# Optimization experiments

Measured on AMD Instinct MI355X. Metric: run time of the kernel, lower is better.

The kernel has to match this reference:

```python
import jax, jax.numpy as jnp
import numpy as np
from jax import lax

ACT_SCALE = (0.5, 0.5, 0.5)  # act_scale[0..2], also used as bias_scale
STRIDE = 2
QLEVELS = 127.0  # int8 fake-quant levels (2**7 - 1)


@jax.custom_vjp
def ste_round(x):
    return jnp.round(x)

def _ste_fwd(x):
    return jnp.round(x), None

def _ste_bwd(_, g):
    return (g,)

ste_round.defvjp(_ste_fwd, _ste_bwd)


def fq_act(x, scale):
    # quantize_activations_gemm_A: normalize by scale, clip to [-1,1], 8-bit grid
    return ste_round(jnp.clip(x / scale, -1.0, 1.0) * QLEVELS) / QLEVELS


def qw(w):
    # quantize_weight_gemm_S: per-tensor max-abs scale + 8-bit fake quant
    s = jnp.max(jnp.abs(w))
    wq = ste_round(jnp.clip(w / s, -1.0, 1.0) * QLEVELS) / QLEVELS
    return wq, s


def qb(b):
    # quantize_bias_gemm: round to 1/127 grid
    return ste_round(b * QLEVELS) / QLEVELS


def relu6s(x, scale):
    # ReLU6S: scaled ReLU6
    return jnp.clip(x / scale, 0.0, 6.0)


def conv(x, w, stride=1, pad=0):
    return lax.conv_general_dilated(
        x, w, (stride, stride), [(pad, pad), (pad, pad)],
        dimension_numbers=("NCHW", "OIHW", "NCHW"))


def bottleneck_fwd(x, w1, b1, w2, b2, w3, b3, ws, bs):
    s0, s1, s2a = ACT_SCALE
    x = fq_act(x, s0)
    residual = x
    # conv1: 1x1
    w1q, c1s = qw(w1)
    b1q = qb(b1) / (c1s * s0)
    out = (conv(x, w1q) + b1q[None, :, None, None]) * c1s
    out = relu6s(out, s0) * s0
    out = fq_act(out, s1)
    # conv2: 3x3 stride
    w2q, c2s = qw(w2)
    b2q = qb(b2) / (c2s * s1)
    out = (conv(out, w2q, stride=STRIDE, pad=1) + b2q[None, :, None, None]) * c2s
    out = relu6s(out, s1) * s1
    out = fq_act(out, s2a)
    # conv3: 1x1 (source's padding=1 on a 1x1 conv is a shape bug; dropped)
    w3q, c3s = qw(w3)
    b3q = qb(b3) / (c2s * s2a)  # NOTE: source divides by conv2_scale (preserved)
    out = (conv(out, w3q) + b3q[None, :, None, None]) * c3s
    out = out * s2a
    # downsample shortcut: 1x1 stride
    wsq, css = qw(ws)
    bsq = qb(bs) / (css * s0)
    residual = (conv(residual, wsq, stride=STRIDE) + bsq[None, :, None, None]) * css
    residual = residual * s0
    return jnp.clip(out + residual, 0.0, 6.0)  # final ReLU6


def setup_inputs() -> dict:
    key = jax.random.key(0)
    ks = jax.random.split(key, 9)
    B, Cin, P, H, W = 64, 512, 256, 28, 28
    Cout = 4 * P
    def w_init(k, shape):
        fan_in = shape[1] * shape[2] * shape[3]
        return jax.random.normal(k, shape, jnp.float32) * np.float32(np.sqrt(2.0 / fan_in))
    return {
        "x": jax.random.normal(ks[0], (B, Cin, H, W), jnp.float32),
        "w1": w_init(ks[1], (P, Cin, 1, 1)),
        "b1": jax.random.normal(ks[2], (P,), jnp.float32) * 0.01,
        "w2": w_init(ks[3], (P, P, 3, 3)),
        "b2": jax.random.normal(ks[4], (P,), jnp.float32) * 0.01,
        "w3": w_init(ks[5], (Cout, P, 1, 1)),
        "b3": jax.random.normal(ks[6], (Cout,), jnp.float32) * 0.01,
        "ws": w_init(ks[7], (Cout, Cin, 1, 1)),
        "bs": jax.random.normal(ks[8], (Cout,), jnp.float32) * 0.01,
    }


def reference(x, w1, b1, w2, b2, w3, b3, ws, bs):
    return bottleneck_fwd(x, w1, b1, w2, b2, w3, b3, ws, bs)
```

## Files before the change

kernel.cpp:

```cpp
#include <hip/hip_runtime.h>
#include <stdint.h>

typedef int   int4v __attribute__((ext_vector_type(4)));
typedef float f32x4 __attribute__((ext_vector_type(4)));

#define WS_SCALES 0ull
#define WS_ZERO   256ull
#define WS_BI1    1024ull
#define WS_BI2    2048ull
#define WS_BI3    4096ull
#define WS_BIS    8192ull
#define WS_W1Q    16384ull
#define WS_W2Q    (WS_W1Q + 131072ull)
#define WS_W3Q    (WS_W2Q + 589824ull)
#define WS_WSQ    (WS_W3Q + 262144ull)
#define WS_A0     2097152ull
#define WS_A1     (WS_A0 + 25690112ull)
#define WS_A2     (WS_A1 + 12845056ull)

__device__ __forceinline__ void gll16(const void* g, void* l) {
    __builtin_amdgcn_global_load_lds((const __attribute__((address_space(1))) void*)g,
                                     (__attribute__((address_space(3))) void*)l, 16, 0, 0);
}

#define VMCNT_BAR(n) asm volatile("s_waitcnt vmcnt(" #n ")\n\ts_barrier" ::: "memory")

__global__ void k_init(float* wshead) {
    int i = blockIdx.x * 256 + threadIdx.x;
    wshead[i] = 0.0f;
}

__global__ void k_maxabs(const float* __restrict__ w1, const float* __restrict__ w2,
                         const float* __restrict__ w3, const float* __restrict__ wsd,
                         float* __restrict__ scales) {
    const float* srcs[4] = {w1, w2, w3, wsd};
    const int ns[4] = {131072, 589824, 262144, 524288};
    int t = blockIdx.y;
    const float* s = srcs[t];
    int n = ns[t];
    float m = 0.0f;
    for (int i = blockIdx.x * 256 + threadIdx.x; i < n; i += gridDim.x * 256)
        m = fmaxf(m, fabsf(s[i]));
    __shared__ float red[256];
    red[threadIdx.x] = m;
    __syncthreads();
    for (int st = 128; st > 0; st >>= 1) {
        if (threadIdx.x < st) red[threadIdx.x] = fmaxf(red[threadIdx.x], red[threadIdx.x + st]);
        __syncthreads();
    }
    if (threadIdx.x == 0) atomicMax((int*)&scales[t], __float_as_int(red[0]));
}

__global__ void k_quant_w(const float* __restrict__ w1, const float* __restrict__ w2,
                          const float* __restrict__ w3, const float* __restrict__ wsd,
                          const float* __restrict__ b1, const float* __restrict__ b2,
                          const float* __restrict__ b3, const float* __restrict__ bs,
                          char* __restrict__ wsb) {
    const float* sc = (const float*)(wsb + WS_SCALES);
    int mode = blockIdx.y;
    int i0 = blockIdx.x * 256 + threadIdx.x;
    int stride = gridDim.x * 256;
    if (mode == 0) {
        float s = sc[0]; signed char* o = (signed char*)(wsb + WS_W1Q);
        for (int i = i0; i < 131072; i += stride)
            o[i] = (signed char)(int)rintf(fminf(fmaxf(w1[i] / s, -1.f), 1.f) * 127.f);
    } else if (mode == 1) {
        float s = sc[1]; signed char* o = (signed char*)(wsb + WS_W2Q);
        for (int i = i0; i < 589824; i += stride) {
            int oo = i / 2304, r2 = i - oo * 2304;
            int c = r2 / 9, kk = r2 - c * 9;
            o[(size_t)oo * 2304 + kk * 256 + c] =
                (signed char)(int)rintf(fminf(fmaxf(w2[i] / s, -1.f), 1.f) * 127.f);
        }
    } else if (mode == 2) {
        float s = sc[2]; signed char* o = (signed char*)(wsb + WS_W3Q);
        for (int i = i0; i < 262144; i += stride)
            o[i] = (signed char)(int)rintf(fminf(fmaxf(w3[i] / s, -1.f), 1.f) * 127.f);
    } else if (mode == 3) {
        float s = sc[3]; signed char* o = (signed char*)(wsb + WS_WSQ);
        for (int i = i0; i < 524288; i += stride)
            o[i] = (signed char)(int)rintf(fminf(fmaxf(wsd[i] / s, -1.f), 1.f) * 127.f);
    } else if (mode == 4) {
        float* o = (float*)(wsb + WS_BI1);
        for (int i = i0; i < 256; i += stride) o[i] = rintf(b1[i] * 127.f);
    } else if (mode == 5) {
        float* o = (float*)(wsb + WS_BI2);
        for (int i = i0; i < 256; i += stride) o[i] = rintf(b2[i] * 127.f);
    } else if (mode == 6) {
        float* o = (float*)(wsb + WS_BI3);
        for (int i = i0; i < 1024; i += stride) o[i] = rintf(b3[i] * 127.f);
    } else {
        float* o = (float*)(wsb + WS_BIS);
        for (int i = i0; i < 1024; i += stride) o[i] = rintf(bs[i] * 127.f);
    }
}

__global__ void k_quant_x(const float* __restrict__ x, signed char* __restrict__ a0) {
    __shared__ signed char tile[32][33];
    int b = blockIdx.z;
    int p0 = blockIdx.x * 32, c0 = blockIdx.y * 32;
    int tp = threadIdx.x & 31, tr = threadIdx.x >> 5;
    const float* xb = x + ((size_t)b * 512 + c0) * 784 + p0;
    for (int i = 0; i < 4; i++) {
        int cc = tr + i * 8;
        float v = (p0 + tp < 784) ? xb[(size_t)cc * 784 + tp] : 0.f;
        v = fminf(fmaxf(v * 2.f, -1.f), 1.f);
        tile[cc][tp] = (signed char)(int)rintf(v * 127.f);
    }
    __syncthreads();
    int pp = threadIdx.x >> 3, cs = (threadIdx.x & 7) * 4;
    if (p0 + pp < 784) {
        unsigned pk = 0;
        for (int i = 0; i < 4; i++)
            pk |= (unsigned)(unsigned char)tile[cs + i][pp] << (8 * i);
        *(unsigned*)(a0 + ((size_t)b * 784 + p0 + pp) * 512 + c0 + cs) = pk;
    }
}

template <int MODE, int BM, int BN, int WGM, int WGN>
__global__ __launch_bounds__(256) void k_conv(char* __restrict__ wsb, float* __restrict__ dout) {
    constexpr int FM = BM / WGM / 16;
    constexpr int FN = BN / WGN / 16;
    constexpr int ISS_A = BM / 16;
    constexpr int NISS = (BM + BN) / 16;
    constexpr int NI = NISS / 4;
    constexpr int KTOT = (MODE == 0) ? 512 : (MODE == 1) ? 2304 : 768;
    constexpr int NSTEP = KTOT / 64;
    constexpr int BMP = BM + 16;
    constexpr int LDS_STAGE = (BM + BN) * 64;
    constexpr int LDS_EPI = (MODE == 2) ? 64 * (BN + 4) * 4 : BN * BMP;
    constexpr int LDSZ = (3 * LDS_STAGE > LDS_EPI) ? 3 * LDS_STAGE : LDS_EPI;

    __shared__ alignas(16) char lds[LDSZ];

    const int tid = threadIdx.x;
    const int wid = tid >> 6;
    const int lane = tid & 63;
    const int n0 = blockIdx.x * BN;
    const int m0 = blockIdx.y * BM;
    const int bb = blockIdx.z;

    const float* sc = (const float*)(wsb + WS_SCALES);
    const int srow = lane >> 2;
    const int lrow = lane & 15;
    const int quad = lane >> 4;
    const int wm = (wid % WGM) * (BM / WGM);
    const int wn = (wid / WGM) * (BN / WGN);
    const int xco = ((lane & 3) ^ ((lane >> 3) & 3)) << 4;
    const char* zp = wsb + WS_ZERO + xco;

    int4v acc3[FM][FN] = {};
    int4v accS[FM][FN] = {};

    auto src_ptr = [&](int s, int k0) -> const char* {
        const char* g;
        if (s < ISS_A) {
            int m = m0 + s * 16 + srow;
            if (MODE == 0)
                g = wsb + WS_W1Q + (size_t)m * 512 + k0 + xco;
            else if (MODE == 1)
                g = wsb + WS_W2Q + (size_t)m * 2304 + k0 + xco;
            else
                g = (k0 < 256) ? wsb + WS_W3Q + (size_t)m * 256 + k0 + xco
                               : wsb + WS_WSQ + (size_t)m * 512 + (k0 - 256) + xco;
        } else {
            int n = n0 + (s - ISS_A) * 16 + srow;
            g = zp;
            if (MODE == 0) {
                g = wsb + WS_A0 + (size_t)n * 512 + k0 + xco;
            } else if (MODE == 1) {
                unsigned b = (unsigned)n / 196u;
                unsigned hw = (unsigned)n - b * 196u;
                int oh = hw / 14, ow = hw - oh * 14;
                int tap = k0 >> 8;
                int kh = tap / 3, kw = tap - kh * 3;
                int c0 = k0 & 255;
                int ih = 2 * oh - 1 + kh, iw = 2 * ow - 1 + kw;
                if (ih >= 0 && ih < 28 && iw >= 0 && iw < 28)
                    g = wsb + WS_A1 + ((size_t)b * 784 + ih * 28 + iw) * 256 + c0 + xco;
            } else {
                if (n < 196) {
                    if (k0 < 256) {
                        g = wsb + WS_A2 + ((size_t)bb * 196 + n) * 256 + k0 + xco;
                    } else {
                        int oh = n / 14, ow = n - oh * 14;
                        int ps = oh * 56 + ow * 2;
                        g = wsb + WS_A0 + ((size_t)bb * 784 + ps) * 512 + (k0 - 256) + xco;
                    }
                }
            }
        }
        return g;
    };

    auto stage = [&](int t, char* buf) {
        const int k0 = t * 64;
#pragma unroll
        for (int ii = 0; ii < NI; ii++) {
            const int s = wid + ii * 4;
            gll16(src_ptr(s, k0), buf + s * 1024);
        }
    };

    stage(0, lds);
    stage(1, lds + LDS_STAGE);
    for (int t = 0; t < NSTEP; ++t) {
        char* cur = lds + (t % 3) * LDS_STAGE;
        if (t == NSTEP - 1) {
            VMCNT_BAR(0);
        } else if constexpr (NI == 3) {
            VMCNT_BAR(3);
        } else {
            VMCNT_BAR(4);
        }
        if (t + 2 < NSTEP) stage(t + 2, lds + ((t + 2) % 3) * LDS_STAGE);

        int4v afr[FM], bfr[FN];
#pragma unroll
        for (int i = 0; i < FM; i++) {
            int m = wm + i * 16 + lrow;
            afr[i] = *(const int4v*)(cur + m * 64 + ((quad ^ ((m >> 1) & 3)) << 4));
        }
#pragma unroll
        for (int j = 0; j < FN; j++) {
            int n = wn + j * 16 + lrow;
            bfr[j] = *(const int4v*)(cur + (BM + n) * 64 + ((quad ^ ((n >> 1) & 3)) << 4));
        }
        if (MODE != 2 || t < 4) {
#pragma unroll
            for (int i = 0; i < FM; i++)
#pragma unroll
                for (int j = 0; j < FN; j++)
                    acc3[i][j] = __builtin_amdgcn_mfma_i32_16x16x64_i8(afr[i], bfr[j], acc3[i][j], 0, 0, 0);
        } else {
#pragma unroll
            for (int i = 0; i < FM; i++)
#pragma unroll
                for (int j = 0; j < FN; j++)
                    accS[i][j] = __builtin_amdgcn_mfma_i32_16x16x64_i8(afr[i], bfr[j], accS[i][j], 0, 0, 0);
        }
    }

    if (MODE == 0 || MODE == 1) {
        const float alpha = sc[MODE] / 16129.0f;
        const float* bi = (const float*)(wsb + (MODE == 0 ? WS_BI1 : WS_BI2));
        signed char* outp = (signed char*)(wsb + (MODE == 0 ? WS_A1 : WS_A2));
        __syncthreads();
#pragma unroll
        for (int i = 0; i < FM; i++) {
            int mloc = wm + i * 16 + quad * 4;
            int mb = m0 + mloc;
            float bt[4];
#pragma unroll
            for (int r = 0; r < 4; r++) bt[r] = bi[mb + r] * (2.0f / 127.0f);
#pragma unroll
            for (int j = 0; j < FN; j++) {
                int nloc = wn + j * 16 + lrow;
                unsigned pk = 0;
#pragma unroll
                for (int r = 0; r < 4; r++) {
                    float v = alpha * (float)acc3[i][j][r] + bt[r];
                    int q = (int)rintf(127.0f * fminf(fmaxf(2.0f * v, 0.0f), 1.0f));
                    pk |= (unsigned)(q & 0xFF) << (8 * r);
                }
                *(unsigned*)(lds + nloc * BMP + mloc) = pk;
            }
        }
        __syncthreads();
        for (int u = tid; u < BN * (BM / 16); u += 256) {
            int row = u / (BM / 16);
            int seg = u % (BM / 16);
            uint4 v = *(const uint4*)(lds + row * BMP + seg * 16);
            *(uint4*)(outp + (size_t)(n0 + row) * 256 + m0 + seg * 16) = v;
        }
    } else {
        const float c2 = sc[1], c3 = sc[2], cS = sc[3];
        const float* bi3 = (const float*)(wsb + WS_BI3);
        const float* bis = (const float*)(wsb + WS_BIS);
        float* ldsF = (float*)lds;
        constexpr int LDN = BN + 4;
        constexpr int SEGS = BN / 16;
        for (int half = 0; half < 2; half++) {
            __syncthreads();
            if (wm == half * 64) {
#pragma unroll
                for (int i = 0; i < FM; i++) {
                    int mloc = i * 16 + quad * 4;
                    int mg = m0 + half * 64 + mloc;
                    float bt[4];
#pragma unroll
                    for (int r = 0; r < 4; r++)
                        bt[r] = bi3[mg + r] * (c3 / (127.0f * c2)) + bis[mg + r] * (1.0f / 127.0f);
#pragma unroll
                    for (int j = 0; j < FN; j++) {
                        int nloc = wn + j * 16 + lrow;
#pragma unroll
                        for (int r = 0; r < 4; r++) {
                            float v = (c3 * (float)acc3[i][j][r] + cS * (float)accS[i][j][r])
                                          * (0.5f / 16129.0f) + bt[r];
                            v = v < 0.0f ? 0.0f : (v > 6.0f ? 6.0f : v);
                            ldsF[(mloc + r) * LDN + nloc] = v;
                        }
                    }
                }
            }
            __syncthreads();
            {
                int rw0 = tid / SEGS, seg = tid % SEGS;
                int nbase = n0 + seg * 16;
                for (int row = rw0; row < 64; row += 256 / SEGS) {
                    const float* src = ldsF + row * LDN + seg * 16;
                    float* dst = dout + ((size_t)bb * 1024 + m0 + half * 64 + row) * 196 + nbase;
                    if (nbase + 16 <= 196) {
                        *(f32x4*)(dst + 0)  = *(const f32x4*)(src + 0);
                        *(f32x4*)(dst + 4)  = *(const f32x4*)(src + 4);
                        *(f32x4*)(dst + 8)  = *(const f32x4*)(src + 8);
                        *(f32x4*)(dst + 12) = *(const f32x4*)(src + 12);
                    } else {
                        for (int q = 0; q < 16 && nbase + q < 196; q++) dst[q] = src[q];
                    }
                }
            }
        }
    }
}

extern "C" void kernel_launch(void* const* d_in, const int* in_sizes, int n_in,
                              void* d_out, int out_size, void* d_ws, size_t ws_size,
                              hipStream_t stream) {
    const float* x   = (const float*)d_in[0];
    const float* w1  = (const float*)d_in[1];
    const float* b1  = (const float*)d_in[2];
    const float* w2  = (const float*)d_in[3];
    const float* b2  = (const float*)d_in[4];
    const float* w3  = (const float*)d_in[5];
    const float* b3  = (const float*)d_in[6];
    const float* wsd = (const float*)d_in[7];
    const float* bs  = (const float*)d_in[8];
    float* out = (float*)d_out;
    char* wsb = (char*)d_ws;

    k_init<<<16, 256, 0, stream>>>((float*)wsb);
    k_maxabs<<<dim3(32, 4), 256, 0, stream>>>(w1, w2, w3, wsd, (float*)(wsb + WS_SCALES));
    k_quant_w<<<dim3(96, 8), 256, 0, stream>>>(w1, w2, w3, wsd, b1, b2, b3, bs, wsb);
    k_quant_x<<<dim3(25, 16, 64), 256, 0, stream>>>(x, (signed char*)(wsb + WS_A0));
    k_conv<0, 128, 128, 2, 2><<<dim3(392, 2, 1), 256, 0, stream>>>(wsb, out);
    k_conv<1, 64, 128, 2, 2><<<dim3(98, 4, 1), 256, 0, stream>>>(wsb, out);
    k_conv<2, 128, 128, 2, 2><<<dim3(2, 8, 64), 256, 0, stream>>>(wsb, out);
}
```

Measured before the change: 328.7 us.

## Load conv weights directly to registers, vectorize quant_x and maxabs

The conv kernels no longer stage the weight (A) operand through LDS. Each wave now loads its A fragments straight from global memory into registers, double-buffered across an unrolled-by-two K loop, and only the activation (B) tiles go through the LDS triple buffer. This cuts LDS footprint and global-to-LDS traffic, at the cost of more registers and uncoalesced 16-byte global loads per lane. Separately, k_quant_x is widened to 128 pixels per block with float4 loads, and k_maxabs uses float4 loads over a larger grid, to reduce memory instruction overhead in the preprocessing.

```diff
diff --git a/kernel.cpp b/kernel.cpp
--- a/kernel.cpp
+++ b/kernel.cpp
@@ -34,13 +34,15 @@
                          const float* __restrict__ w3, const float* __restrict__ wsd,
                          float* __restrict__ scales) {
     const float* srcs[4] = {w1, w2, w3, wsd};
-    const int ns[4] = {131072, 589824, 262144, 524288};
+    const int n4s[4] = {32768, 147456, 65536, 131072};
     int t = blockIdx.y;
-    const float* s = srcs[t];
-    int n = ns[t];
+    const f32x4* s = (const f32x4*)srcs[t];
+    int n4 = n4s[t];
     float m = 0.0f;
-    for (int i = blockIdx.x * 256 + threadIdx.x; i < n; i += gridDim.x * 256)
-        m = fmaxf(m, fabsf(s[i]));
+    for (int i = blockIdx.x * 256 + threadIdx.x; i < n4; i += gridDim.x * 256) {
+        f32x4 v = s[i];
+        m = fmaxf(m, fmaxf(fmaxf(fabsf(v[0]), fabsf(v[1])), fmaxf(fabsf(v[2]), fabsf(v[3]))));
+    }
     __shared__ float red[256];
     red[threadIdx.x] = m;
     __syncthreads();
@@ -95,25 +97,39 @@
     }
 }
 
-__global__ void k_quant_x(const float* __restrict__ x, signed char* __restrict__ a0) {
-    __shared__ signed char tile[32][33];
+__global__ __launch_bounds__(256) void k_quant_x(const float* __restrict__ x,
+                                                 signed char* __restrict__ a0) {
+    __shared__ signed char tile[32][132];
     int b = blockIdx.z;
-    int p0 = blockIdx.x * 32, c0 = blockIdx.y * 32;
-    int tp = threadIdx.x & 31, tr = threadIdx.x >> 5;
-    const float* xb = x + ((size_t)b * 512 + c0) * 784 + p0;
-    for (int i = 0; i < 4; i++) {
-        int cc = tr + i * 8;
-        float v = (p0 + tp < 784) ? xb[(size_t)cc * 784 + tp] : 0.f;
-        v = fminf(fmaxf(v * 2.f, -1.f), 1.f);
-        tile[cc][tp] = (signed char)(int)rintf(v * 127.f);
+    int p0 = blockIdx.x * 128, c0 = blockIdx.y * 32;
+    int tc = threadIdx.x >> 3;
+    int pq = (threadIdx.x & 7) * 16;
+    const float* xr = x + ((size_t)b * 512 + c0 + tc) * 784 + p0 + pq;
+#pragma unroll
+    for (int u = 0; u < 4; u++) {
+        int p = p0 + pq + u * 4;
+        f32x4 v = {0.f, 0.f, 0.f, 0.f};
+        if (p < 784) v = *(const f32x4*)(xr + u * 4);
+        signed char q[4];
+#pragma unroll
+        for (int e = 0; e < 4; e++) {
+            float f = fminf(fmaxf(v[e] * 2.f, -1.f), 1.f);
+            q[e] = (signed char)(int)rintf(f * 127.f);
+        }
+        *(int*)&tile[tc][pq + u * 4] = *(int*)q;
     }
     __syncthreads();
-    int pp = threadIdx.x >> 3, cs = (threadIdx.x & 7) * 4;
-    if (p0 + pp < 784) {
-        unsigned pk = 0;
-        for (int i = 0; i < 4; i++)
-            pk |= (unsigned)(unsigned char)tile[cs + i][pp] << (8 * i);
-        *(unsigned*)(a0 + ((size_t)b * 784 + p0 + pp) * 512 + c0 + cs) = pk;
+#pragma unroll
+    for (int u = 0; u < 4; u++) {
+        int idx = threadIdx.x + u * 256;
+        int pp = idx >> 3, cs = (idx & 7) * 4;
+        if (p0 + pp < 784) {
+            unsigned pk = 0;
+#pragma unroll
+            for (int i = 0; i < 4; i++)
+                pk |= (unsigned)(unsigned char)tile[cs + i][pp] << (8 * i);
+            *(unsigned*)(a0 + ((size_t)b * 784 + p0 + pp) * 512 + c0 + cs) = pk;
+        }
     }
 }
 
@@ -121,15 +137,17 @@
 __global__ __launch_bounds__(256) void k_conv(char* __restrict__ wsb, float* __restrict__ dout) {
     constexpr int FM = BM / WGM / 16;
     constexpr int FN = BN / WGN / 16;
-    constexpr int ISS_A = BM / 16;
-    constexpr int NISS = (BM + BN) / 16;
-    constexpr int NI = NISS / 4;
+    constexpr int SB = BN / 16;
+    constexpr int NI_B = SB / 4;
     constexpr int KTOT = (MODE == 0) ? 512 : (MODE == 1) ? 2304 : 768;
     constexpr int NSTEP = KTOT / 64;
     constexpr int BMP = BM + 16;
-    constexpr int LDS_STAGE = (BM + BN) * 64;
+    constexpr int LDS_STAGE = BN * 64;
     constexpr int LDS_EPI = (MODE == 2) ? 64 * (BN + 4) * 4 : BN * BMP;
     constexpr int LDSZ = (3 * LDS_STAGE > LDS_EPI) ? 3 * LDS_STAGE : LDS_EPI;
+    static_assert(FM + NI_B == 6 || FM + NI_B == 4, "steady bar count");
+    static_assert(FM == 4 || FM == 2, "tail bar count");
+    static_assert(NSTEP % 2 == 0, "even steps");
 
     __shared__ alignas(16) char lds[LDSZ];
 
@@ -149,99 +167,125 @@
     const int xco = ((lane & 3) ^ ((lane >> 3) & 3)) << 4;
     const char* zp = wsb + WS_ZERO + xco;
 
+    const char* aB[FM];
+    const char* aB2[FM];
+#pragma unroll
+    for (int i = 0; i < FM; i++) {
+        int m = m0 + wm + i * 16 + lrow;
+        if constexpr (MODE == 0) {
+            aB[i] = wsb + WS_W1Q + (size_t)m * 512 + quad * 16;
+        } else if constexpr (MODE == 1) {
+            aB[i] = wsb + WS_W2Q + (size_t)m * 2304 + quad * 16;
+        } else {
+            aB[i]  = wsb + WS_W3Q + (size_t)m * 256 + quad * 16;
+            aB2[i] = wsb + WS_WSQ + (size_t)m * 512 + quad * 16;
+        }
+    }
+
     int4v acc3[FM][FN] = {};
     int4v accS[FM][FN] = {};
 
-    auto src_ptr = [&](int s, int k0) -> const char* {
-        const char* g;
-        if (s < ISS_A) {
-            int m = m0 + s * 16 + srow;
-            if (MODE == 0)
-                g = wsb + WS_W1Q + (size_t)m * 512 + k0 + xco;
-            else if (MODE == 1)
-                g = wsb + WS_W2Q + (size_t)m * 2304 + k0 + xco;
-            else
-                g = (k0 < 256) ? wsb + WS_W3Q + (size_t)m * 256 + k0 + xco
-                               : wsb + WS_WSQ + (size_t)m * 512 + (k0 - 256) + xco;
+    auto srcB = [&](int s, int k0) -> const char* {
+        int n = n0 + s * 16 + srow;
+        const char* g = zp;
+        if constexpr (MODE == 0) {
+            g = wsb + WS_A0 + (size_t)n * 512 + k0 + xco;
+        } else if constexpr (MODE == 1) {
+            unsigned b = (unsigned)n / 196u;
+            unsigned hw = (unsigned)n - b * 196u;
+            int oh = hw / 14, ow = hw - oh * 14;
+            int tap = k0 >> 8;
+            int kh = tap / 3, kw = tap - kh * 3;
+            int c0 = k0 & 255;
+            int ih = 2 * oh - 1 + kh, iw = 2 * ow - 1 + kw;
+            if (ih >= 0 && ih < 28 && iw >= 0 && iw < 28)
+                g = wsb + WS_A1 + ((size_t)b * 784 + ih * 28 + iw) * 256 + c0 + xco;
         } else {
-            int n = n0 + (s - ISS_A) * 16 + srow;
-            g = zp;
-            if (MODE == 0) {
-                g = wsb + WS_A0 + (size_t)n * 512 + k0 + xco;
-            } else if (MODE == 1) {
-                unsigned b = (unsigned)n / 196u;
-                unsigned hw = (unsigned)n - b * 196u;
-                int oh = hw / 14, ow = hw - oh * 14;
-                int tap = k0 >> 8;
-                int kh = tap / 3, kw = tap - kh * 3;
-                int c0 = k0 & 255;
-                int ih = 2 * oh - 1 + kh, iw = 2 * ow - 1 + kw;
-                if (ih >= 0 && ih < 28 && iw >= 0 && iw < 28)
-                    g = wsb + WS_A1 + ((size_t)b * 784 + ih * 28 + iw) * 256 + c0 + xco;
+            if (n < 196) {
+                if (k0 < 256) {
+                    g = wsb + WS_A2 + ((size_t)bb * 196 + n) * 256 + k0 + xco;
+                } else {
+                    int oh = n / 14, ow = n - oh * 14;
+                    int ps = oh * 56 + ow * 2;
+                    g = wsb + WS_A0 + ((size_t)bb * 784 + ps) * 512 + (k0 - 256) + xco;
+                }
+            }
+        }
+        return g;
+    };
+
+    auto stageB = [&](int t, char* buf) {
+        const int k0 = t * 64;
+#pragma unroll
+        for (int ii = 0; ii < NI_B; ii++) {
+            const int s = wid + ii * 4;
+            gll16(srcB(s, k0), buf + s * 1024);
+        }
+    };
+
+    auto loadA = [&](int t, int4v (&a)[FM]) {
+        if constexpr (MODE == 2) {
+            if (t < 4) {
+                const int off = t * 64;
+#pragma unroll
+                for (int i = 0; i < FM; i++) a[i] = *(const int4v*)(aB[i] + off);
             } else {
-                if (n < 196) {
-                    if (k0 < 256) {
-                        g = wsb + WS_A2 + ((size_t)bb * 196 + n) * 256 + k0 + xco;
-                    } else {
-                        int oh = n / 14, ow = n - oh * 14;
-                        int ps = oh * 56 + ow * 2;
-                        g = wsb + WS_A0 + ((size_t)bb * 784 + ps) * 512 + (k0 - 256) + xco;
-                    }
-                }
-            }
-        }
-        return g;
-    };
-
-    auto stage = [&](int t, char* buf) {
-        const int k0 = t * 64;
-#pragma unroll
-        for (int ii = 0; ii < NI; ii++) {
-            const int s = wid + ii * 4;
-            gll16(src_ptr(s, k0), buf + s * 1024);
-        }
-    };
-
-    stage(0, lds);
-    stage(1, lds + LDS_STAGE);
-    for (int t = 0; t < NSTEP; ++t) {
-        char* cur = lds + (t % 3) * LDS_STAGE;
-        if (t == NSTEP - 1) {
-            VMCNT_BAR(0);
-        } else if constexpr (NI == 3) {
-            VMCNT_BAR(3);
+                const int off = (t - 4) * 64;
+#pragma unroll
+                for (int i = 0; i < FM; i++) a[i] = *(const int4v*)(aB2[i] + off);
+            }
         } else {
-            VMCNT_BAR(4);
-        }
-        if (t + 2 < NSTEP) stage(t + 2, lds + ((t + 2) % 3) * LDS_STAGE);
-
-        int4v afr[FM], bfr[FN];
-#pragma unroll
-        for (int i = 0; i < FM; i++) {
-            int m = wm + i * 16 + lrow;
-            afr[i] = *(const int4v*)(cur + m * 64 + ((quad ^ ((m >> 1) & 3)) << 4));
-        }
+            const int off = t * 64;
+#pragma unroll
+            for (int i = 0; i < FM; i++) a[i] = *(const int4v*)(aB[i] + off);
+        }
+    };
+
+    auto dsB = [&](const char* cur, int4v (&b)[FN]) {
 #pragma unroll
         for (int j = 0; j < FN; j++) {
             int n = wn + j * 16 + lrow;
-            bfr[j] = *(const int4v*)(cur + (BM + n) * 64 + ((quad ^ ((n >> 1) & 3)) << 4));
-        }
-        if (MODE != 2 || t < 4) {
-#pragma unroll
-            for (int i = 0; i < FM; i++)
-#pragma unroll
-                for (int j = 0; j < FN; j++)
-                    acc3[i][j] = __builtin_amdgcn_mfma_i32_16x16x64_i8(afr[i], bfr[j], acc3[i][j], 0, 0, 0);
+            b[j] = *(const int4v*)(cur + n * 64 + ((quad ^ ((n >> 1) & 3)) << 4));
+        }
+    };
+
+    auto MF = [&](int4v (&ac)[FM][FN], int4v (&a)[FM], int4v (&b)[FN]) {
+#pragma unroll
+        for (int i = 0; i < FM; i++)
+#pragma unroll
+            for (int j = 0; j < FN; j++)
+                ac[i][j] = __builtin_amdgcn_mfma_i32_16x16x64_i8(a[i], b[j], ac[i][j], 0, 0, 0);
+    };
+
+    int4v aC[FM], aN[FM], bfr[FN];
+    stageB(0, lds);
+    stageB(1, lds + LDS_STAGE);
+    loadA(0, aC);
+    VMCNT_BAR(0);
+
+    for (int t = 0; t < NSTEP; t += 2) {
+        loadA(t + 1, aN);
+        __builtin_amdgcn_sched_barrier(0);
+        if (t + 2 < NSTEP) stageB(t + 2, lds + ((t + 2) % 3) * LDS_STAGE);
+        dsB(lds + (t % 3) * LDS_STAGE, bfr);
+        if (MODE != 2 || t < 4) MF(acc3, aC, bfr); else MF(accS, aC, bfr);
+        if (t + 1 == NSTEP - 1) {
+            if constexpr (FM == 4) VMCNT_BAR(4); else VMCNT_BAR(2);
         } else {
-#pragma unroll
-            for (int i = 0; i < FM; i++)
-#pragma unroll
-                for (int j = 0; j < FN; j++)
-                    accS[i][j] = __builtin_amdgcn_mfma_i32_16x16x64_i8(afr[i], bfr[j], accS[i][j], 0, 0, 0);
-        }
-    }
-
-    if (MODE == 0 || MODE == 1) {
+            if constexpr (FM + NI_B == 6) VMCNT_BAR(6); else VMCNT_BAR(4);
+        }
+
+        if (t + 2 < NSTEP) loadA(t + 2, aC);
+        __builtin_amdgcn_sched_barrier(0);
+        if (t + 3 < NSTEP) stageB(t + 3, lds + ((t + 3) % 3) * LDS_STAGE);
+        dsB(lds + ((t + 1) % 3) * LDS_STAGE, bfr);
+        if (MODE != 2 || t + 1 < 4) MF(acc3, aN, bfr); else MF(accS, aN, bfr);
+        if (t + 2 < NSTEP) {
+            if constexpr (FM + NI_B == 6) VMCNT_BAR(6); else VMCNT_BAR(4);
+        }
+    }
+
+    if constexpr (MODE == 0 || MODE == 1) {
         const float alpha = sc[MODE] / 16129.0f;
         const float* bi = (const float*)(wsb + (MODE == 0 ? WS_BI1 : WS_BI2));
         signed char* outp = (signed char*)(wsb + (MODE == 0 ? WS_A1 : WS_A2));
@@ -341,9 +385,9 @@
     char* wsb = (char*)d_ws;
 
     k_init<<<16, 256, 0, stream>>>((float*)wsb);
-    k_maxabs<<<dim3(32, 4), 256, 0, stream>>>(w1, w2, w3, wsd, (float*)(wsb + WS_SCALES));
+    k_maxabs<<<dim3(128, 4), 256, 0, stream>>>(w1, w2, w3, wsd, (float*)(wsb + WS_SCALES));
     k_quant_w<<<dim3(96, 8), 256, 0, stream>>>(w1, w2, w3, wsd, b1, b2, b3, bs, wsb);
-    k_quant_x<<<dim3(25, 16, 64), 256, 0, stream>>>(x, (signed char*)(wsb + WS_A0));
+    k_quant_x<<<dim3(7, 16, 64), 256, 0, stream>>>(x, (signed char*)(wsb + WS_A0));
     k_conv<0, 128, 128, 2, 2><<<dim3(392, 2, 1), 256, 0, stream>>>(wsb, out);
     k_conv<1, 64, 128, 2, 2><<<dim3(98, 4, 1), 256, 0, stream>>>(wsb, out);
     k_conv<2, 128, 128, 2, 2><<<dim3(2, 8, 64), 256, 0, stream>>>(wsb, out);
```

Measured after the change: 334.9 us. About the same (+1.9%).

## Shrink conv tiles to 64x64, vectorize maxabs and input quantization

Applied to the files above, without the earlier changes.

All three conv kernels now use 64x64 tiles with launch bounds of four blocks per CU. This multiplies the grid size to raise occupancy and simplifies the epilogues into single-pass stores. The maxabs and input-quantization kernels are vectorized with float4 loads, and quant_x now processes 128 pixels per block. The barrier macro also waits on lgkmcnt(0). Smaller tiles reduce data reuse per block and increase global and LDS traffic.

```diff
diff --git a/kernel.cpp b/kernel.cpp
--- a/kernel.cpp
+++ b/kernel.cpp
@@ -23,7 +23,7 @@
                                      (__attribute__((address_space(3))) void*)l, 16, 0, 0);
 }
 
-#define VMCNT_BAR(n) asm volatile("s_waitcnt vmcnt(" #n ")\n\ts_barrier" ::: "memory")
+#define VMCNT_BAR(n) asm volatile("s_waitcnt vmcnt(" #n ") lgkmcnt(0)\n\ts_barrier" ::: "memory")
 
 __global__ void k_init(float* wshead) {
     int i = blockIdx.x * 256 + threadIdx.x;
@@ -34,13 +34,15 @@
                          const float* __restrict__ w3, const float* __restrict__ wsd,
                          float* __restrict__ scales) {
     const float* srcs[4] = {w1, w2, w3, wsd};
-    const int ns[4] = {131072, 589824, 262144, 524288};
+    const int n4s[4] = {32768, 147456, 65536, 131072};
     int t = blockIdx.y;
-    const float* s = srcs[t];
-    int n = ns[t];
+    const f32x4* s = (const f32x4*)srcs[t];
+    int n4 = n4s[t];
     float m = 0.0f;
-    for (int i = blockIdx.x * 256 + threadIdx.x; i < n; i += gridDim.x * 256)
-        m = fmaxf(m, fabsf(s[i]));
+    for (int i = blockIdx.x * 256 + threadIdx.x; i < n4; i += gridDim.x * 256) {
+        f32x4 v = s[i];
+        m = fmaxf(m, fmaxf(fmaxf(fabsf(v[0]), fabsf(v[1])), fmaxf(fabsf(v[2]), fabsf(v[3]))));
+    }
     __shared__ float red[256];
     red[threadIdx.x] = m;
     __syncthreads();
@@ -95,41 +97,53 @@
     }
 }
 
-__global__ void k_quant_x(const float* __restrict__ x, signed char* __restrict__ a0) {
-    __shared__ signed char tile[32][33];
+__global__ __launch_bounds__(256) void k_quant_x(const float* __restrict__ x,
+                                                 signed char* __restrict__ a0) {
+    __shared__ signed char tile[32][132];
     int b = blockIdx.z;
-    int p0 = blockIdx.x * 32, c0 = blockIdx.y * 32;
-    int tp = threadIdx.x & 31, tr = threadIdx.x >> 5;
-    const float* xb = x + ((size_t)b * 512 + c0) * 784 + p0;
-    for (int i = 0; i < 4; i++) {
-        int cc = tr + i * 8;
-        float v = (p0 + tp < 784) ? xb[(size_t)cc * 784 + tp] : 0.f;
-        v = fminf(fmaxf(v * 2.f, -1.f), 1.f);
-        tile[cc][tp] = (signed char)(int)rintf(v * 127.f);
+    int p0 = blockIdx.x * 128, c0 = blockIdx.y * 32;
+    int tc = threadIdx.x >> 3;
+    int pq = (threadIdx.x & 7) * 16;
+    const float* xr = x + ((size_t)b * 512 + c0 + tc) * 784 + p0 + pq;
+#pragma unroll
+    for (int u = 0; u < 4; u++) {
+        int p = p0 + pq + u * 4;
+        f32x4 v = {0.f, 0.f, 0.f, 0.f};
+        if (p < 784) v = *(const f32x4*)(xr + u * 4);
+        signed char q[4];
+#pragma unroll
+        for (int e = 0; e < 4; e++) {
+            float f = fminf(fmaxf(v[e] * 2.f, -1.f), 1.f);
+            q[e] = (signed char)(int)rintf(f * 127.f);
+        }
+        *(int*)&tile[tc][pq + u * 4] = *(int*)q;
     }
     __syncthreads();
-    int pp = threadIdx.x >> 3, cs = (threadIdx.x & 7) * 4;
-    if (p0 + pp < 784) {
-        unsigned pk = 0;
-        for (int i = 0; i < 4; i++)
-            pk |= (unsigned)(unsigned char)tile[cs + i][pp] << (8 * i);
-        *(unsigned*)(a0 + ((size_t)b * 784 + p0 + pp) * 512 + c0 + cs) = pk;
-    }
-}
-
-template <int MODE, int BM, int BN, int WGM, int WGN>
-__global__ __launch_bounds__(256) void k_conv(char* __restrict__ wsb, float* __restrict__ dout) {
-    constexpr int FM = BM / WGM / 16;
-    constexpr int FN = BN / WGN / 16;
+#pragma unroll
+    for (int u = 0; u < 4; u++) {
+        int idx = threadIdx.x + u * 256;
+        int pp = idx >> 3, cs = (idx & 7) * 4;
+        if (p0 + pp < 784) {
+            unsigned pk = 0;
+#pragma unroll
+            for (int i = 0; i < 4; i++)
+                pk |= (unsigned)(unsigned char)tile[cs + i][pp] << (8 * i);
+            *(unsigned*)(a0 + ((size_t)b * 784 + p0 + pp) * 512 + c0 + cs) = pk;
+        }
+    }
+}
+
+template <int MODE>
+__global__ __launch_bounds__(256, 4) void k_conv(char* __restrict__ wsb, float* __restrict__ dout) {
+    constexpr int BM = 64, BN = 64, WGM = 2;
+    constexpr int FM = 2, FN = 2;
     constexpr int ISS_A = BM / 16;
-    constexpr int NISS = (BM + BN) / 16;
-    constexpr int NI = NISS / 4;
+    constexpr int NI = (BM + BN) / 64;
     constexpr int KTOT = (MODE == 0) ? 512 : (MODE == 1) ? 2304 : 768;
     constexpr int NSTEP = KTOT / 64;
     constexpr int BMP = BM + 16;
     constexpr int LDS_STAGE = (BM + BN) * 64;
-    constexpr int LDS_EPI = (MODE == 2) ? 64 * (BN + 4) * 4 : BN * BMP;
-    constexpr int LDSZ = (3 * LDS_STAGE > LDS_EPI) ? 3 * LDS_STAGE : LDS_EPI;
+    constexpr int LDSZ = 3 * LDS_STAGE;
 
     __shared__ alignas(16) char lds[LDSZ];
 
@@ -145,7 +159,7 @@
     const int lrow = lane & 15;
     const int quad = lane >> 4;
     const int wm = (wid % WGM) * (BM / WGM);
-    const int wn = (wid / WGM) * (BN / WGN);
+    const int wn = (wid / WGM) * (BN / WGM);
     const int xco = ((lane & 3) ^ ((lane >> 3) & 3)) << 4;
     const char* zp = wsb + WS_ZERO + xco;
 
@@ -208,10 +222,8 @@
         char* cur = lds + (t % 3) * LDS_STAGE;
         if (t == NSTEP - 1) {
             VMCNT_BAR(0);
-        } else if constexpr (NI == 3) {
-            VMCNT_BAR(3);
         } else {
-            VMCNT_BAR(4);
+            VMCNT_BAR(2);
         }
         if (t + 2 < NSTEP) stage(t + 2, lds + ((t + 2) % 3) * LDS_STAGE);
 
@@ -241,7 +253,7 @@
         }
     }
 
-    if (MODE == 0 || MODE == 1) {
+    if constexpr (MODE == 0 || MODE == 1) {
         const float alpha = sc[MODE] / 16129.0f;
         const float* bi = (const float*)(wsb + (MODE == 0 ? WS_BI1 : WS_BI2));
         signed char* outp = (signed char*)(wsb + (MODE == 0 ? WS_A1 : WS_A2));
@@ -267,9 +279,8 @@
             }
         }
         __syncthreads();
-        for (int u = tid; u < BN * (BM / 16); u += 256) {
-            int row = u / (BM / 16);
-            int seg = u % (BM / 16);
+        {
+            int row = tid >> 2, seg = tid & 3;
             uint4 v = *(const uint4*)(lds + row * BMP + seg * 16);
             *(uint4*)(outp + (size_t)(n0 + row) * 256 + m0 + seg * 16) = v;
         }
@@ -279,47 +290,40 @@
         const float* bis = (const float*)(wsb + WS_BIS);
         float* ldsF = (float*)lds;
         constexpr int LDN = BN + 4;
-        constexpr int SEGS = BN / 16;
-        for (int half = 0; half < 2; half++) {
-            __syncthreads();
-            if (wm == half * 64) {
-#pragma unroll
-                for (int i = 0; i < FM; i++) {
-                    int mloc = i * 16 + quad * 4;
-                    int mg = m0 + half * 64 + mloc;
-                    float bt[4];
-#pragma unroll
-                    for (int r = 0; r < 4; r++)
-                        bt[r] = bi3[mg + r] * (c3 / (127.0f * c2)) + bis[mg + r] * (1.0f / 127.0f);
-#pragma unroll
-                    for (int j = 0; j < FN; j++) {
-                        int nloc = wn + j * 16 + lrow;
-#pragma unroll
-                        for (int r = 0; r < 4; r++) {
-                            float v = (c3 * (float)acc3[i][j][r] + cS * (float)accS[i][j][r])
-                                          * (0.5f / 16129.0f) + bt[r];
-                            v = v < 0.0f ? 0.0f : (v > 6.0f ? 6.0f : v);
-                            ldsF[(mloc + r) * LDN + nloc] = v;
-                        }
-                    }
+        __syncthreads();
+#pragma unroll
+        for (int i = 0; i < FM; i++) {
+            int mloc = wm + i * 16 + quad * 4;
+            int mg = m0 + mloc;
+            float bt[4];
+#pragma unroll
+            for (int r = 0; r < 4; r++)
+                bt[r] = bi3[mg + r] * (c3 / (127.0f * c2)) + bis[mg + r] * (1.0f / 127.0f);
+#pragma unroll
+            for (int j = 0; j < FN; j++) {
+                int nloc = wn + j * 16 + lrow;
+#pragma unroll
+                for (int r = 0; r < 4; r++) {
+                    float v = (c3 * (float)acc3[i][j][r] + cS * (float)accS[i][j][r])
+                                  * (0.5f / 16129.0f) + bt[r];
+                    v = v < 0.0f ? 0.0f : (v > 6.0f ? 6.0f : v);
+                    ldsF[(mloc + r) * LDN + nloc] = v;
                 }
             }
-            __syncthreads();
-            {
-                int rw0 = tid / SEGS, seg = tid % SEGS;
-                int nbase = n0 + seg * 16;
-                for (int row = rw0; row < 64; row += 256 / SEGS) {
-                    const float* src = ldsF + row * LDN + seg * 16;
-                    float* dst = dout + ((size_t)bb * 1024 + m0 + half * 64 + row) * 196 + nbase;
-                    if (nbase + 16 <= 196) {
-                        *(f32x4*)(dst + 0)  = *(const f32x4*)(src + 0);
-                        *(f32x4*)(dst + 4)  = *(const f32x4*)(src + 4);
-                        *(f32x4*)(dst + 8)  = *(const f32x4*)(src + 8);
-                        *(f32x4*)(dst + 12) = *(const f32x4*)(src + 12);
-                    } else {
-                        for (int q = 0; q < 16 && nbase + q < 196; q++) dst[q] = src[q];
-                    }
-                }
+        }
+        __syncthreads();
+        {
+            int row = tid >> 2, seg = tid & 3;
+            int nbase = n0 + seg * 16;
+            const float* src = ldsF + row * LDN + seg * 16;
+            float* dst = dout + ((size_t)bb * 1024 + m0 + row) * 196 + nbase;
+            if (nbase + 16 <= 196) {
+                *(f32x4*)(dst + 0)  = *(const f32x4*)(src + 0);
+                *(f32x4*)(dst + 4)  = *(const f32x4*)(src + 4);
+                *(f32x4*)(dst + 8)  = *(const f32x4*)(src + 8);
+                *(f32x4*)(dst + 12) = *(const f32x4*)(src + 12);
+            } else {
+                for (int q = 0; q < 16 && nbase + q < 196; q++) dst[q] = src[q];
             }
         }
     }
@@ -341,10 +345,10 @@
     char* wsb = (char*)d_ws;
 
     k_init<<<16, 256, 0, stream>>>((float*)wsb);
-    k_maxabs<<<dim3(32, 4), 256, 0, stream>>>(w1, w2, w3, wsd, (float*)(wsb + WS_SCALES));
+    k_maxabs<<<dim3(128, 4), 256, 0, stream>>>(w1, w2, w3, wsd, (float*)(wsb + WS_SCALES));
     k_quant_w<<<dim3(96, 8), 256, 0, stream>>>(w1, w2, w3, wsd, b1, b2, b3, bs, wsb);
-    k_quant_x<<<dim3(25, 16, 64), 256, 0, stream>>>(x, (signed char*)(wsb + WS_A0));
-    k_conv<0, 128, 128, 2, 2><<<dim3(392, 2, 1), 256, 0, stream>>>(wsb, out);
-    k_conv<1, 64, 128, 2, 2><<<dim3(98, 4, 1), 256, 0, stream>>>(wsb, out);
-    k_conv<2, 128, 128, 2, 2><<<dim3(2, 8, 64), 256, 0, stream>>>(wsb, out);
-}
+    k_quant_x<<<dim3(7, 16, 64), 256, 0, stream>>>(x, (signed char*)(wsb + WS_A0));
+    k_conv<0><<<dim3(784, 4, 1), 256, 0, stream>>>(wsb, out);
+    k_conv<1><<<dim3(196, 4, 1), 256, 0, stream>>>(wsb, out);
+    k_conv<2><<<dim3(4, 16, 64), 256, 0, stream>>>(wsb, out);
+}
```

After: 299.8 us. -8.8%, faster.
